# Kernel tuning notes

Hardware: AMD Instinct MI355X
Metric: run time of the kernel (lower is better)

The kernel has to match this reference:

```python
import jax, jax.numpy as jnp
import numpy as np

B, N, K, DEG = 512, 128, 8, 16
NR = 200            # num_rels (padding idx = NR)
INP, SEM, EMB, L = 32, 16, 32, 3
FEAT = INP - SEM
NN = B * N
E = NN * DEG
OUT = L * EMB       # 96


def _gru_cell(x, h, Wih, Whh, bih, bhh):
    gi = x @ Wih.T + bih
    gh = h @ Whh.T + bhh
    ir, iz, i_n = jnp.split(gi, 3, axis=-1)
    hr, hz, hn = jnp.split(gh, 3, axis=-1)
    r = jax.nn.sigmoid(ir + hr)
    z = jax.nn.sigmoid(iz + hz)
    n = jnp.tanh(i_n + r * hn)
    return (1.0 - z) * n + z * h


def _run_gru(xs, h0, Wih, Whh, bih, bhh):
    # xs: [T, batch, in]
    def step(h, x):
        h2 = _gru_cell(x, h, Wih, Whh, bih, bhh)
        return h2, h2
    hT, ys = jax.lax.scan(step, h0, xs)
    return ys, hT


def _forward(feat, out_nei_rels, in_nei_rels, r_label_node, src, dst, etype, rel_labels,
             rel_emb, w_rel2ent_W, w_rel2ent_b, W_msg, W_self, b_gnn, W_rel,
             gru_bias, gru_Wih_f, gru_Whh_f, gru_bih_f, gru_bhh_f,
             gru_Wih_b, gru_Whh_b, gru_bih_b, gru_bhh_b,
             Wo_W, Wo_b, path_Wih, path_Whh, path_bih, path_bhh, fc_W, fc_b):
    # --- init_ent_emb_matrix: neighbor-relation attention vs target relation ---
    out_e = rel_emb[out_nei_rels]                      # [NN,K,INP]
    in_e = rel_emb[in_nei_rels]                        # [NN,K,INP]
    tgt = rel_emb[r_label_node]                        # [NN,INP]
    out_att = jax.nn.softmax(jnp.einsum('nkd,nd->nk', out_e, tgt), axis=1)
    in_att = jax.nn.softmax(jnp.einsum('nkd,nd->nk', in_e, tgt), axis=1)
    out_sem = jnp.einsum('nk,nkd->nd', out_att, out_e)
    in_sem = jnp.einsum('nk,nkd->nd', in_att, in_e)
    sem = jax.nn.sigmoid(jnp.concatenate([out_sem, in_sem], axis=1) @ w_rel2ent_W + w_rel2ent_b)
    h = jnp.concatenate([feat, sem], axis=1)           # [NN,INP]

    # --- RGCN-style relational message passing; repr = concat of layer outputs ---
    r = rel_emb
    deg = jnp.maximum(jax.ops.segment_sum(jnp.ones((E,), h.dtype), dst, NN), 1.0)[:, None]
    reprs = []
    for l in range(L):
        msg = h[src] * r[etype]                        # [E,EMB]  (gather-heavy)
        agg = jax.ops.segment_sum(msg, dst, NN) / deg  # mean aggregation
        h = jax.nn.relu(agg @ W_msg[l] + h @ W_self[l] + b_gnn[l])
        r = r @ W_rel[l]                               # relation stream (padding row stays 0)
        reprs.append(h)
    repr_ = jnp.concatenate(reprs, axis=1)             # [NN,OUT]
    r_emb_out = r                                      # [NR+1,EMB]

    # --- BatchGRU: bidirectional GRU over each graph's node sequence ---
    node = repr_.reshape(B, N, OUT)
    message = jax.nn.relu(node + gru_bias)
    h0 = jnp.max(node, axis=1)                         # per-graph max init hidden
    xs = jnp.swapaxes(message, 0, 1)                   # [N,B,OUT]
    ys_f, _ = _run_gru(xs, h0, gru_Wih_f, gru_Whh_f, gru_bih_f, gru_bhh_f)
    ys_b, _ = _run_gru(xs[::-1], h0, gru_Wih_b, gru_Whh_b, gru_bih_b, gru_bhh_b)
    gru_out = jnp.concatenate([ys_f, ys_b[::-1]], axis=-1)  # [N,B,2*OUT]
    repr2 = jax.nn.relu(jnp.swapaxes(gru_out, 0, 1).reshape(NN, 2 * OUT))
    node_hidden = jax.nn.relu(repr2 @ Wo_W + Wo_b)     # [NN,OUT]

    nh = node_hidden.reshape(B, N, OUT)
    g_out = jnp.mean(nh, axis=1)                       # mean_nodes
    head_embs = nh[:, 0]                               # node id==1 is node 0 of each graph
    tail_embs = nh[:, 1]                               # node id==2 is node 1 of each graph

    # --- nei_rel_path: GRU over (h_r, r_t, t_r) triples, attention aggregation ---
    in_rels = in_nei_rels.reshape(B, N, K)
    heads_rels = in_rels[:, 0]                         # [B,K]
    tails_rels = in_rels[:, 1]                         # [B,K]
    P = K * K
    paths = jnp.stack([
        jnp.repeat(heads_rels, K, axis=1),
        jnp.broadcast_to(rel_labels[:, None], (B, P)),
        jnp.tile(tails_rels, (1, K)),
    ], axis=-1).reshape(B * P, 3)
    pe = r_emb_out[paths]                              # [B*P,3,EMB]
    _, last = _run_gru(jnp.swapaxes(pe, 0, 1), jnp.zeros((B * P, EMB), pe.dtype),
                       path_Wih, path_Whh, path_bih, path_bhh)
    last = last.reshape(B, P, EMB)
    r_lab_e = r_emb_out[rel_labels]                    # [B,EMB]
    atts = jax.nn.softmax(jnp.einsum('bpe,be->bp', last, r_lab_e), axis=1)
    g_p = jnp.einsum('bp,bpe->be', atts, last)         # [B,EMB]

    g_rep = jnp.concatenate([g_out, head_embs, tail_embs, r_lab_e, g_p], axis=1)  # [B,352]
    return g_rep @ fc_W + fc_b                         # [B,1]


def setup_inputs():
    key = jax.random.key(0)
    ks = jax.random.split(key, 40)
    idx = iter(range(40))
    def nk():
        return ks[next(idx)]
    def _p(shape, scale=0.1):
        return jax.random.normal(nk(), shape, jnp.float32) * scale

    feat = jax.random.normal(nk(), (NN, FEAT), jnp.float32)
    out_nei_rels = jax.random.randint(nk(), (NN, K), 0, NR)
    in_nei_rels = jax.random.randint(nk(), (NN, K), 0, NR)
    rel_labels = jax.random.randint(nk(), (B,), 0, NR)
    r_label_node = jnp.repeat(rel_labels, N)
    gid = jnp.arange(E) // (N * DEG)                   # edges stay within their graph
    src = gid * N + jax.random.randint(nk(), (E,), 0, N)
    dst = gid * N + jax.random.randint(nk(), (E,), 0, N)
    etype = jax.random.randint(nk(), (E,), 0, NR)
    rel_emb = jax.random.normal(nk(), (NR + 1, INP), jnp.float32) * 0.5
    rel_emb = rel_emb.at[NR].set(0.0)                  # padding_idx row

    return {
        'feat': feat, 'out_nei_rels': out_nei_rels, 'in_nei_rels': in_nei_rels,
        'r_label_node': r_label_node, 'src': src, 'dst': dst, 'etype': etype,
        'rel_labels': rel_labels, 'rel_emb': rel_emb,
        'w_rel2ent_W': _p((2 * INP, SEM)), 'w_rel2ent_b': _p((SEM,)),
        'W_msg': _p((L, EMB, EMB)), 'W_self': _p((L, EMB, EMB)),
        'b_gnn': _p((L, EMB)), 'W_rel': _p((L, INP, INP)),
        'gru_bias': _p((OUT,)),
        'gru_Wih_f': _p((3 * OUT, OUT)), 'gru_Whh_f': _p((3 * OUT, OUT)),
        'gru_bih_f': _p((3 * OUT,)), 'gru_bhh_f': _p((3 * OUT,)),
        'gru_Wih_b': _p((3 * OUT, OUT)), 'gru_Whh_b': _p((3 * OUT, OUT)),
        'gru_bih_b': _p((3 * OUT,)), 'gru_bhh_b': _p((3 * OUT,)),
        'Wo_W': _p((2 * OUT, OUT)), 'Wo_b': _p((OUT,)),
        'path_Wih': _p((3 * EMB, EMB)), 'path_Whh': _p((3 * EMB, EMB)),
        'path_bih': _p((3 * EMB,)), 'path_bhh': _p((3 * EMB,)),
        'fc_W': _p((3 * OUT + 2 * EMB, 1)), 'fc_b': _p((1,)),
    }


def reference(feat, out_nei_rels, in_nei_rels, r_label_node, src, dst, etype, rel_labels,
              rel_emb, w_rel2ent_W, w_rel2ent_b, W_msg, W_self, b_gnn, W_rel,
              gru_bias, gru_Wih_f, gru_Whh_f, gru_bih_f, gru_bhh_f,
              gru_Wih_b, gru_Whh_b, gru_bih_b, gru_bhh_b,
              Wo_W, Wo_b, path_Wih, path_Whh, path_bih, path_bhh, fc_W, fc_b):
    return _forward(feat, out_nei_rels, in_nei_rels, r_label_node, src, dst, etype, rel_labels,
                    rel_emb, w_rel2ent_W, w_rel2ent_b, W_msg, W_self, b_gnn, W_rel,
                    gru_bias, gru_Wih_f, gru_Whh_f, gru_bih_f, gru_bhh_f,
                    gru_Wih_b, gru_Whh_b, gru_bih_b, gru_bhh_b,
                    Wo_W, Wo_b, path_Wih, path_Whh, path_bih, path_bhh, fc_W, fc_b)
```

## Files before the change

### kernel.cpp

```cpp
#include <hip/hip_runtime.h>
#include <math.h>

#define BB 512
#define NT 128
#define NREL 201
#define NNODE (BB*NT)
#define NEDGE (NNODE*16)

typedef float f32x4 __attribute__((ext_vector_type(4)));
typedef __attribute__((ext_vector_type(8))) short bf16x8;

__device__ __forceinline__ float sigm(float x) { return 1.f/(1.f + __expf(-x)); }

__device__ __forceinline__ unsigned short f2bf(float f) {
  unsigned u; __builtin_memcpy(&u, &f, 4);
  unsigned r = u + 0x7fffu + ((u >> 16) & 1u);
  return (unsigned short)(r >> 16);
}

__global__ __launch_bounds__(96) void k_rel2(const float* __restrict__ rel_emb,
                                             const float* __restrict__ W_rel,
                                             const float* __restrict__ pWih,
                                             const float* __restrict__ pbih,
                                             float* __restrict__ r123,
                                             float* __restrict__ XI) {
  __shared__ float ra[32], rb[32];
  int r = blockIdx.x, tid = threadIdx.x;
  if (tid < 32) ra[tid] = rel_emb[r*32 + tid];
  __syncthreads();
  if (tid < 32) {
    float s = 0.f;
    #pragma unroll
    for (int d = 0; d < 32; ++d) s += ra[d]*W_rel[d*32 + tid];
    rb[tid] = s; r123[0*NREL*32 + r*32 + tid] = s;
  }
  __syncthreads();
  if (tid < 32) {
    float s = 0.f;
    #pragma unroll
    for (int d = 0; d < 32; ++d) s += rb[d]*W_rel[1024 + d*32 + tid];
    ra[tid] = s; r123[1*NREL*32 + r*32 + tid] = s;
  }
  __syncthreads();
  if (tid < 32) {
    float s = 0.f;
    #pragma unroll
    for (int d = 0; d < 32; ++d) s += ra[d]*W_rel[2048 + d*32 + tid];
    rb[tid] = s; r123[2*NREL*32 + r*32 + tid] = s;
  }
  __syncthreads();
  float s = pbih[tid];
  #pragma unroll
  for (int d = 0; d < 32; ++d) s += rb[d]*pWih[tid*32 + d];
  XI[r*96 + tid] = s;
}

__global__ __launch_bounds__(256) void k_wt1(const float* __restrict__ Wih_f,
                                             const float* __restrict__ Wih_b,
                                             const float* __restrict__ bih_f,
                                             const float* __restrict__ bih_b,
                                             unsigned short* __restrict__ WT1bt,
                                             float* __restrict__ bcat) {
  int i = blockIdx.x*256 + threadIdx.x;
  if (i < 576*96) {
    int j = i / 96;
    float v = (j < 288) ? Wih_f[i] : Wih_b[i - 288*96];
    WT1bt[i] = f2bf(v);
  }
  if (i < 576) bcat[i] = (i < 288) ? bih_f[i] : bih_b[i-288];
}

__device__ __forceinline__ void sem_att(const float* __restrict__ rel_emb,
                                        const int rels[8], const float tgt[32],
                                        float out[32]) {
  float dots[8]; float mx = -1e30f;
  #pragma unroll
  for (int k = 0; k < 8; ++k) {
    const float4* er = (const float4*)(rel_emb + rels[k]*32);
    float s = 0.f;
    #pragma unroll
    for (int q = 0; q < 8; ++q) {
      float4 v = er[q];
      s += v.x*tgt[4*q+0] + v.y*tgt[4*q+1] + v.z*tgt[4*q+2] + v.w*tgt[4*q+3];
    }
    dots[k] = s; mx = fmaxf(mx, s);
  }
  float den = 0.f;
  #pragma unroll
  for (int k = 0; k < 8; ++k) { float e = __expf(dots[k]-mx); dots[k] = e; den += e; }
  float inv = 1.f/den;
  #pragma unroll
  for (int d = 0; d < 32; ++d) out[d] = 0.f;
  #pragma unroll
  for (int k = 0; k < 8; ++k) {
    const float4* er = (const float4*)(rel_emb + rels[k]*32);
    float a = dots[k]*inv;
    #pragma unroll
    for (int q = 0; q < 8; ++q) {
      float4 v = er[q];
      out[4*q+0] += a*v.x; out[4*q+1] += a*v.y; out[4*q+2] += a*v.z; out[4*q+3] += a*v.w;
    }
  }
}

__global__ __launch_bounds__(256) void k_sem(
    const float* __restrict__ feat, const int* __restrict__ out_rels,
    const int* __restrict__ in_rels, const int* __restrict__ r_label_node,
    const float* __restrict__ rel_emb, const float* __restrict__ W,
    const float* __restrict__ bias, float* __restrict__ hin) {
  int n = blockIdx.x*256 + threadIdx.x;
  float tgt[32];
  {
    const float4* tr = (const float4*)(rel_emb + r_label_node[n]*32);
    #pragma unroll
    for (int q = 0; q < 8; ++q) {
      float4 v = tr[q];
      tgt[4*q+0]=v.x; tgt[4*q+1]=v.y; tgt[4*q+2]=v.z; tgt[4*q+3]=v.w;
    }
  }
  int ro[8], ri[8];
  #pragma unroll
  for (int k = 0; k < 8; ++k) { ro[k] = out_rels[n*8+k]; ri[k] = in_rels[n*8+k]; }
  float osem[32], isem[32];
  sem_att(rel_emb, ro, tgt, osem);
  sem_att(rel_emb, ri, tgt, isem);
  const float4* fr = (const float4*)(feat + (size_t)n*16);
  float4* ho = (float4*)(hin + (size_t)n*32);
  #pragma unroll
  for (int q = 0; q < 4; ++q) ho[q] = fr[q];
  #pragma unroll
  for (int j = 0; j < 16; ++j) {
    float s = bias[j];
    #pragma unroll
    for (int d = 0; d < 32; ++d) s += osem[d]*W[d*16+j] + isem[d]*W[(32+d)*16+j];
    hin[(size_t)n*32 + 16 + j] = sigm(s);
  }
}

__global__ __launch_bounds__(512) void k_gnn3(
    const float* __restrict__ hin, const float* __restrict__ rel_emb,
    const float* __restrict__ r123,
    const int* __restrict__ src, const int* __restrict__ dst, const int* __restrict__ etype,
    const float* __restrict__ W_msg, const float* __restrict__ W_self,
    const float* __restrict__ b_gnn,
    float* __restrict__ AT, float* __restrict__ ghid0) {
  __shared__ __align__(16) float hl[NT*36];
  __shared__ __align__(16) float hnew[NT*33];
  __shared__ float rl[NREL*32];
  __shared__ unsigned short eidx[2048];
  __shared__ float scratch[16][32];
  __shared__ int cnt[128], fill[128], scanv[128], rowstart[129];
  int g = blockIdx.x;
  int tid = threadIdx.x;
  int d = tid & 31, grp = tid >> 5;

  for (int i = tid; i < NT*32; i += 512) {
    int row = i >> 5, col = i & 31;
    hl[row*36 + col] = hin[(size_t)(g*NT + row)*32 + col];
  }
  if (tid < 128) { cnt[tid] = 0; fill[tid] = 0; }
  __syncthreads();
  for (int i = tid; i < 2048; i += 512)
    atomicAdd(&cnt[dst[g*2048 + i] - g*NT], 1);
  __syncthreads();
  if (tid < 128) scanv[tid] = cnt[tid];
  __syncthreads();
  #pragma unroll
  for (int off = 1; off < 128; off <<= 1) {
    int v = 0;
    if (tid < 128 && tid >= off) v = scanv[tid - off];
    __syncthreads();
    if (tid < 128) scanv[tid] += v;
    __syncthreads();
  }
  if (tid < 128) { rowstart[tid+1] = scanv[tid]; if (tid == 0) rowstart[0] = 0; }
  __syncthreads();
  for (int i = tid; i < 2048; i += 512) {
    int e = g*2048 + i;
    int dl = dst[e] - g*NT;
    int slot = rowstart[dl] + atomicAdd(&fill[dl], 1);
    eidx[slot] = (unsigned short)(((src[e] - g*NT) << 8) | etype[e]);
  }

  for (int l = 0; l < 3; ++l) {
    const float* rsrc = (l == 0) ? rel_emb : (r123 + (size_t)(l-1)*NREL*32);
    for (int i = tid; i < NREL*32; i += 512) rl[i] = rsrc[i];
    float wm[32], ws[32];
    #pragma unroll
    for (int dd = 0; dd < 32; ++dd) {
      wm[dd] = W_msg[l*1024 + dd*32 + d];
      ws[dd] = W_self[l*1024 + dd*32 + d];
    }
    float bj = b_gnn[l*32 + d];
    __syncthreads();
    for (int k2 = 0; k2 < 8; ++k2) {
      int n = grp + k2*16;
      int e0 = rowstart[n], e1 = rowstart[n+1];
      float acc = 0.f;
      for (int e = e0; e < e1; ++e) {
        int pk = eidx[e];
        acc += hl[(pk >> 8)*36 + d] * rl[(pk & 255)*32 + d];
      }
      scratch[grp][d] = acc;
      float invd = 1.f / (float)((e1 - e0) > 0 ? (e1 - e0) : 1);
      float sa = 0.f, sh = 0.f;
      #pragma unroll
      for (int dd = 0; dd < 32; ++dd) {
        sa += scratch[grp][dd]*wm[dd];
        sh += hl[n*36 + dd]*ws[dd];
      }
      hnew[n*33 + d] = fmaxf(bj + invd*sa + sh, 0.f);
    }
    __syncthreads();
    for (int i = tid; i < NT*32; i += 512) {
      int row = i >> 5, col = i & 31;
      hl[row*36 + col] = hnew[row*33 + col];
    }
    #pragma unroll
    for (int pass = 0; pass < 8; ++pass) {
      int col = (pass << 2) + (tid >> 7);
      int row = tid & 127;
      AT[(size_t)(l*32 + col)*NNODE + g*NT + row] = hnew[row*33 + col];
    }
    {
      float m = -1e30f;
      #pragma unroll
      for (int k2 = 0; k2 < 8; ++k2) m = fmaxf(m, hnew[(grp + k2*16)*33 + d]);
      scratch[grp][d] = m;
    }
    __syncthreads();
    if (tid < 32) {
      float m = -1e30f;
      #pragma unroll
      for (int p2 = 0; p2 < 16; ++p2) m = fmaxf(m, scratch[p2][tid]);
      ghid0[g*96 + l*32 + tid] = m;
    }
    __syncthreads();
  }
}

__global__ __launch_bounds__(256) void k_gemm1m(
    const float* __restrict__ AT, const float* __restrict__ gbias,
    const unsigned short* __restrict__ WT1bt, const float* __restrict__ bcat,
    float* __restrict__ GI) {
  __shared__ unsigned short As[128*104];
  int m0 = blockIdx.x * 128;
  int tid = threadIdx.x;
  for (int i = tid; i < 96*32; i += 256) {
    int r = i >> 5, c4 = i & 31;
    float4 v = *(const float4*)&AT[(size_t)r*NNODE + m0 + c4*4];
    float b = gbias[r];
    float o0 = fmaxf(v.x+b,0.f), o1 = fmaxf(v.y+b,0.f);
    float o2 = fmaxf(v.z+b,0.f), o3 = fmaxf(v.w+b,0.f);
    As[(c4*4+0)*104 + r] = f2bf(o0);
    As[(c4*4+1)*104 + r] = f2bf(o1);
    As[(c4*4+2)*104 + r] = f2bf(o2);
    As[(c4*4+3)*104 + r] = f2bf(o3);
  }
  __syncthreads();
  int w = tid >> 6, l = tid & 63;
  int lr = l & 15, lh = l >> 4;
  bf16x8 afr[2][3];
  #pragma unroll
  for (int tm = 0; tm < 2; ++tm)
    #pragma unroll
    for (int kc = 0; kc < 3; ++kc)
      afr[tm][kc] = *(const bf16x8*)&As[((w*2+tm)*16 + lr)*104 + kc*32 + lh*8];
  for (int nb = 0; nb < 9; ++nb) {
    int n0 = nb*64;
    #pragma unroll
    for (int tn = 0; tn < 4; ++tn) {
      int col = n0 + tn*16 + lr;
      const unsigned short* bp = WT1bt + (size_t)col*96 + lh*8;
      bf16x8 b0 = *(const bf16x8*)(bp);
      bf16x8 b1 = *(const bf16x8*)(bp + 32);
      bf16x8 b2 = *(const bf16x8*)(bp + 64);
      float bb = bcat[col];
      #pragma unroll
      for (int tm = 0; tm < 2; ++tm) {
        f32x4 acc = {bb, bb, bb, bb};
        acc = __builtin_amdgcn_mfma_f32_16x16x32_bf16(afr[tm][0], b0, acc, 0, 0, 0);
        acc = __builtin_amdgcn_mfma_f32_16x16x32_bf16(afr[tm][1], b1, acc, 0, 0, 0);
        acc = __builtin_amdgcn_mfma_f32_16x16x32_bf16(afr[tm][2], b2, acc, 0, 0, 0);
        int rbase = m0 + (w*2+tm)*16 + lh*4;
        #pragma unroll
        for (int r = 0; r < 4; ++r)
          __builtin_nontemporal_store(acc[r], &GI[(size_t)(rbase + r)*576 + col]);
      }
    }
  }
}

#define PIN4(v) asm volatile("" : "+v"(v.x), "+v"(v.y), "+v"(v.z), "+v"(v.w))
#define DOT16(acc, W0,W1,W2,W3, X0,X1,X2,X3) \
  acc += W0.x*X0.x + W0.y*X0.y + W0.z*X0.z + W0.w*X0.w \
       + W1.x*X1.x + W1.y*X1.y + W1.z*X1.z + W1.w*X1.w \
       + W2.x*X2.x + W2.y*X2.y + W2.z*X2.z + W2.w*X2.w \
       + W3.x*X3.x + W3.y*X3.y + W3.z*X3.z + W3.w*X3.w

__global__ __launch_bounds__(576, 1) void k_gru(
    const float* __restrict__ Whh_f, const float* __restrict__ bhh_f,
    const float* __restrict__ Whh_b, const float* __restrict__ bhh_b,
    const float* __restrict__ GI, const float* __restrict__ ghid0,
    float* __restrict__ AT2) {
  __shared__ __align__(16) float h_lds[4][96];
  __shared__ float part[4][288][9];
  int bx = blockIdx.x;
  int dir = bx >> 7;
  int gbase = (bx & 127) * 4;
  int tid = threadIdx.x;
  int c = tid % 96;
  int p = tid / 96;
  bool fin = (tid < 384);
  int s = p;

  const float* Whh = dir ? Whh_b : Whh_f;
  const float4* wr0 = (const float4*)(Whh + (size_t)c*96 + p*16);
  const float4* wr1 = (const float4*)(Whh + (size_t)(96+c)*96 + p*16);
  const float4* wr2 = (const float4*)(Whh + (size_t)(192+c)*96 + p*16);
  float4 wa0=wr0[0], wa1=wr0[1], wa2=wr0[2], wa3=wr0[3];
  float4 wb0=wr1[0], wb1=wr1[1], wb2=wr1[2], wb3=wr1[3];
  float4 wc0=wr2[0], wc1=wr2[1], wc2=wr2[2], wc3=wr2[3];

  float bh0=0.f, bh1=0.f, bh2=0.f;
  float gi0=0.f, gi1=0.f, gi2=0.f;
  if (fin) {
    const float* bhh = dir ? bhh_b : bhh_f;
    bh0 = bhh[c]; bh1 = bhh[96+c]; bh2 = bhh[192+c];
    h_lds[s][c] = ghid0[(gbase+s)*96 + c];
    int pos0 = dir ? 127 : 0;
    const float* g = GI + (size_t)((gbase+s)*128 + pos0)*576 + dir*288;
    gi0 = g[c]; gi1 = g[96+c]; gi2 = g[192+c];
  }
  __syncthreads();
  for (int t = 0; t < 128; ++t) {
    PIN4(wa0); PIN4(wa1); PIN4(wa2); PIN4(wa3);
    PIN4(wb0); PIN4(wb1); PIN4(wb2); PIN4(wb3);
    PIN4(wc0); PIN4(wc1); PIN4(wc2); PIN4(wc3);
    int pos = dir ? (127-t) : t;
    float gn0=0.f, gn1=0.f, gn2=0.f;
    if (fin && t < 127) {
      int posn = dir ? (126-t) : (t+1);
      const float* g = GI + (size_t)((gbase+s)*128 + posn)*576 + dir*288;
      gn0 = g[c]; gn1 = g[96+c]; gn2 = g[192+c];
    }
    #pragma unroll
    for (int s4 = 0; s4 < 4; ++s4) {
      const float4* hh = (const float4*)&h_lds[s4][p*16];
      float4 x0=hh[0], x1=hh[1], x2=hh[2], x3=hh[3];
      float q0=0.f, q1=0.f, q2=0.f;
      DOT16(q0, wa0,wa1,wa2,wa3, x0,x1,x2,x3);
      DOT16(q1, wb0,wb1,wb2,wb3, x0,x1,x2,x3);
      DOT16(q2, wc0,wc1,wc2,wc3, x0,x1,x2,x3);
      part[s4][c][p]     = q0;
      part[s4][96+c][p]  = q1;
      part[s4][192+c][p] = q2;
    }
    __syncthreads();
    if (fin) {
      const float* pr = part[s][c];
      const float* pz = part[s][96+c];
      const float* pn = part[s][192+c];
      float ghr = pr[0]+pr[1]+pr[2]+pr[3]+pr[4]+pr[5] + bh0;
      float ghz = pz[0]+pz[1]+pz[2]+pz[3]+pz[4]+pz[5] + bh1;
      float ghn = pn[0]+pn[1]+pn[2]+pn[3]+pn[4]+pn[5] + bh2;
      float r  = sigm(gi0 + ghr);
      float z  = sigm(gi1 + ghz);
      float nn = tanhf(gi2 + r*ghn);
      float hv = (1.f - z)*nn + z*h_lds[s][c];
      h_lds[s][c] = hv;
      AT2[(size_t)(dir*96 + c)*NNODE + (gbase+s)*128 + pos] = fmaxf(hv, 0.f);
      gi0 = gn0; gi1 = gn1; gi2 = gn2;
    }
    __syncthreads();
  }
}

__global__ __launch_bounds__(384) void k_gemm2p(
    const float* __restrict__ AT2, const float* __restrict__ WoW,
    const float* __restrict__ Wob, float* __restrict__ goutb,
    float* __restrict__ headb, float* __restrict__ tailb) {
  __shared__ __align__(16) float As[96*64];
  __shared__ __align__(16) float Bs[96*96];
  __shared__ float red[16][100];
  int m0 = blockIdx.x*64;
  int g = m0 >> 7;
  int tid = threadIdx.x;
  int tc = tid % 24, tr = tid / 24;
  int r0 = tr*4, c0 = tc*4;
  float acc[4][4] = {};
  for (int kc = 0; kc < 2; ++kc) {
    for (int i = tid; i < 1536; i += 384) {
      int r = i >> 4, c4 = i & 15;
      *(float4*)&As[r*64 + c4*4] = *(const float4*)&AT2[(size_t)(kc*96 + r)*NNODE + m0 + c4*4];
    }
    for (int i = tid; i < 2304; i += 384) {
      int r = i / 24, c4 = i % 24;
      *(float4*)&Bs[r*96 + c4*4] = *(const float4*)&WoW[(size_t)(kc*96 + r)*96 + c4*4];
    }
    __syncthreads();
    #pragma unroll 8
    for (int k = 0; k < 96; ++k) {
      float4 a = *(float4*)&As[k*64 + r0];
      float4 b = *(float4*)&Bs[k*96 + c0];
      acc[0][0] += a.x*b.x; acc[0][1] += a.x*b.y; acc[0][2] += a.x*b.z; acc[0][3] += a.x*b.w;
      acc[1][0] += a.y*b.x; acc[1][1] += a.y*b.y; acc[1][2] += a.y*b.z; acc[1][3] += a.y*b.w;
      acc[2][0] += a.z*b.x; acc[2][1] += a.z*b.y; acc[2][2] += a.z*b.z; acc[2][3] += a.z*b.w;
      acc[3][0] += a.w*b.x; acc[3][1] += a.w*b.y; acc[3][2] += a.w*b.z; acc[3][3] += a.w*b.w;
    }
    __syncthreads();
  }
  float4 bia = *(const float4*)&Wob[c0];
  float nv[4][4];
  #pragma unroll
  for (int r = 0; r < 4; ++r) {
    nv[r][0] = fmaxf(acc[r][0]+bia.x, 0.f);
    nv[r][1] = fmaxf(acc[r][1]+bia.y, 0.f);
    nv[r][2] = fmaxf(acc[r][2]+bia.z, 0.f);
    nv[r][3] = fmaxf(acc[r][3]+bia.w, 0.f);
  }
  #pragma unroll
  for (int cj = 0; cj < 4; ++cj)
    red[tr][c0+cj] = nv[0][cj] + nv[1][cj] + nv[2][cj] + nv[3][cj];
  if ((m0 & 127) == 0 && tr == 0) {
    #pragma unroll
    for (int cj = 0; cj < 4; ++cj) {
      headb[g*96 + c0 + cj] = nv[0][cj];
      tailb[g*96 + c0 + cj] = nv[1][cj];
    }
  }
  __syncthreads();
  if (tid < 96) {
    float s = 0.f;
    #pragma unroll
    for (int t2 = 0; t2 < 16; ++t2) s += red[t2][tid];
    atomicAdd(&goutb[g*96 + tid], s);
  }
}

__global__ __launch_bounds__(128) void k_path(
    const float* __restrict__ XI, const int* __restrict__ in_rels,
    const int* __restrict__ labels, const float* __restrict__ pWhh,
    const float* __restrict__ pbhh, float* __restrict__ last) {
  __shared__ __align__(16) float wsh[96*32];
  __shared__ float bsh[96];
  __shared__ float hbuf[128*33];
  int tid = threadIdx.x;
  for (int i = tid; i < 96*32; i += 128) wsh[i] = pWhh[i];
  if (tid < 96) bsh[tid] = pbhh[tid];
  int p = blockIdx.x*128 + tid;
  int b = p >> 6, pp = p & 63;
  int rid0 = in_rels[b*1024 + (pp >> 3)];
  int rid1 = labels[b];
  int rid2 = in_rels[b*1024 + 8 + (pp & 7)];
  __syncthreads();
  float* hs = &hbuf[tid*33];
  {
    const float* xi = XI + rid0*96;
    #pragma unroll
    for (int gg = 0; gg < 32; ++gg) {
      float r = sigm(xi[gg] + bsh[gg]);
      float z = sigm(xi[32+gg] + bsh[32+gg]);
      float nn = tanhf(xi[64+gg] + r*bsh[64+gg]);
      hs[gg] = (1.f - z)*nn;
    }
  }
  float4 h4[8];
  #pragma unroll
  for (int q = 0; q < 8; ++q) h4[q] = make_float4(hs[4*q], hs[4*q+1], hs[4*q+2], hs[4*q+3]);
  for (int s = 0; s < 2; ++s) {
    const float* xi = XI + (s == 0 ? rid1 : rid2)*96;
    for (int gg = 0; gg < 32; ++gg) {
      float ar = bsh[gg], az = bsh[32+gg], an = bsh[64+gg];
      const float4* wr = (const float4*)&wsh[gg*32];
      const float4* wz = (const float4*)&wsh[(32+gg)*32];
      const float4* wn = (const float4*)&wsh[(64+gg)*32];
      #pragma unroll
      for (int q = 0; q < 8; ++q) {
        float4 hv = h4[q]; float4 w;
        w = wr[q]; ar += hv.x*w.x + hv.y*w.y + hv.z*w.z + hv.w*w.w;
        w = wz[q]; az += hv.x*w.x + hv.y*w.y + hv.z*w.z + hv.w*w.w;
        w = wn[q]; an += hv.x*w.x + hv.y*w.y + hv.z*w.z + hv.w*w.w;
      }
      float r = sigm(xi[gg] + ar);
      float z = sigm(xi[32+gg] + az);
      float nn = tanhf(xi[64+gg] + r*an);
      hs[gg] = (1.f - z)*nn + z*hs[gg];
    }
    #pragma unroll
    for (int q = 0; q < 8; ++q) h4[q] = make_float4(hs[4*q], hs[4*q+1], hs[4*q+2], hs[4*q+3]);
  }
  float* lp = last + (size_t)p*32;
  #pragma unroll
  for (int d = 0; d < 32; ++d) lp[d] = hs[d];
}

__global__ __launch_bounds__(64) void k_final(
    const float* __restrict__ last, const float* __restrict__ r3,
    const int* __restrict__ labels, const float* __restrict__ goutb,
    const float* __restrict__ headb, const float* __restrict__ tailb,
    const float* __restrict__ fcW, const float* __restrict__ fcb,
    float* __restrict__ out) {
  __shared__ float red[64*33];
  __shared__ float gpl[32];
  int b = blockIdx.x, lane = threadIdx.x;
  const float* rl = r3 + labels[b]*32;
  float l32[32];
  {
    const float4* lr = (const float4*)(last + (size_t)(b*64 + lane)*32);
    #pragma unroll
    for (int q = 0; q < 8; ++q) {
      float4 v = lr[q];
      l32[4*q+0]=v.x; l32[4*q+1]=v.y; l32[4*q+2]=v.z; l32[4*q+3]=v.w;
    }
  }
  float s = 0.f;
  #pragma unroll
  for (int d = 0; d < 32; ++d) s += l32[d]*rl[d];
  float mx = s;
  #pragma unroll
  for (int off = 32; off > 0; off >>= 1) mx = fmaxf(mx, __shfl_xor(mx, off));
  float e = __expf(s - mx);
  float den = e;
  #pragma unroll
  for (int off = 32; off > 0; off >>= 1) den += __shfl_xor(den, off);
  float att = e / den;
  #pragma unroll
  for (int d = 0; d < 32; ++d) red[lane*33 + d] = att*l32[d];
  __syncthreads();
  if (lane < 32) {
    float gp = 0.f;
    for (int p2 = 0; p2 < 64; ++p2) gp += red[p2*33 + lane];
    gpl[lane] = gp;
  }
  __syncthreads();
  float acc = 0.f;
  for (int i = lane; i < 352; i += 64) {
    float v;
    if (i < 96)       v = goutb[b*96 + i] * 0.0078125f;
    else if (i < 192) v = headb[b*96 + (i-96)];
    else if (i < 288) v = tailb[b*96 + (i-192)];
    else if (i < 320) v = rl[i-288];
    else              v = gpl[i-320];
    acc += v*fcW[i];
  }
  #pragma unroll
  for (int off = 32; off > 0; off >>= 1) acc += __shfl_xor(acc, off);
  if (lane == 0) out[b] = acc + fcb[0];
}

extern "C" void kernel_launch(void* const* d_in, const int* in_sizes, int n_in,
                              void* d_out, int out_size, void* d_ws, size_t ws_size,
                              hipStream_t stream) {
  const float* feat       = (const float*)d_in[0];
  const int*   out_rels   = (const int*)d_in[1];
  const int*   in_rels    = (const int*)d_in[2];
  const int*   r_label_nd = (const int*)d_in[3];
  const int*   src        = (const int*)d_in[4];
  const int*   dst        = (const int*)d_in[5];
  const int*   etype      = (const int*)d_in[6];
  const int*   rel_labels = (const int*)d_in[7];
  const float* rel_emb    = (const float*)d_in[8];
  const float* w2e_W      = (const float*)d_in[9];
  const float* w2e_b      = (const float*)d_in[10];
  const float* W_msg      = (const float*)d_in[11];
  const float* W_self     = (const float*)d_in[12];
  const float* b_gnn      = (const float*)d_in[13];
  const float* W_rel      = (const float*)d_in[14];
  const float* gru_bias   = (const float*)d_in[15];
  const float* Wih_f      = (const float*)d_in[16];
  const float* Whh_f      = (const float*)d_in[17];
  const float* bih_f      = (const float*)d_in[18];
  const float* bhh_f      = (const float*)d_in[19];
  const float* Wih_b      = (const float*)d_in[20];
  const float* Whh_b      = (const float*)d_in[21];
  const float* bih_b      = (const float*)d_in[22];
  const float* bhh_b      = (const float*)d_in[23];
  const float* Wo_W       = (const float*)d_in[24];
  const float* Wo_b       = (const float*)d_in[25];
  const float* pWih       = (const float*)d_in[26];
  const float* pWhh       = (const float*)d_in[27];
  const float* pbih       = (const float*)d_in[28];
  const float* pbhh       = (const float*)d_in[29];
  const float* fcW        = (const float*)d_in[30];
  const float* fcb        = (const float*)d_in[31];
  float* out = (float*)d_out;

  float* p = (float*)d_ws;
  float* hin   = p; p += (size_t)NNODE*32;
  float* R1    = p; p += (size_t)NNODE*192;
  float* AT    = R1;
  float* AT2   = R1;
  float* R2    = p; p += (size_t)NNODE*576;
  float* GI    = R2;
  float* r123  = p; p += 3*NREL*32;
  unsigned short* WT1bt = (unsigned short*)p; p += (576*96)/2;
  float* bcat  = p; p += 576;
  float* XI    = p; p += NREL*96;
  float* ghid0 = p; p += BB*96;
  float* goutb = p; p += BB*96;
  float* headb = p; p += BB*96;
  float* tailb = p; p += BB*96;
  float* lastb = p; p += (size_t)BB*64*32;

  hipMemsetAsync(goutb, 0, BB*96*sizeof(float), stream);
  k_rel2<<<NREL, 96, 0, stream>>>(rel_emb, W_rel, pWih, pbih, r123, XI);
  k_wt1<<<(576*96+255)/256, 256, 0, stream>>>(Wih_f, Wih_b, bih_f, bih_b, WT1bt, bcat);
  k_sem<<<NNODE/256, 256, 0, stream>>>(feat, out_rels, in_rels, r_label_nd,
                                       rel_emb, w2e_W, w2e_b, hin);
  k_gnn3<<<BB, 512, 0, stream>>>(hin, rel_emb, r123, src, dst, etype,
                                 W_msg, W_self, b_gnn, AT, ghid0);
  k_gemm1m<<<512, 256, 0, stream>>>(AT, gru_bias, WT1bt, bcat, GI);
  k_gru<<<256, 576, 0, stream>>>(Whh_f, bhh_f, Whh_b, bhh_b, GI, ghid0, AT2);
  k_gemm2p<<<1024, 384, 0, stream>>>(AT2, Wo_W, Wo_b, goutb, headb, tailb);
  k_path<<<256, 128, 0, stream>>>(XI, in_rels, rel_labels, pWhh, pbhh, lastb);
  k_final<<<BB, 64, 0, stream>>>(lastb, r123 + 2*NREL*32, rel_labels,
                                 goutb, headb, tailb, fcW, fcb, out);
}
```

Baseline: 504.0 us.

## Run GRU recurrence on MFMA with split-bf16 weights and interleaved gate layout

The bidirectional GRU hidden-state matmul moves from scalar FP32 dot products with an LDS partial-sum reduction to bf16 MFMA instructions. Weights and hidden state are split into hi/lo bf16 pairs (three MFMA passes) to keep near-FP32 accuracy. The input-gate GEMM now writes its outputs with the r/z/n gates interleaved per channel, so each lane loads all three with one vector load. Each block now handles 16 sequences instead of 4, giving 64 blocks instead of 256. That removes one barrier per step but leaves most CUs idle and adds a weight-prep kernel.

```diff
diff --git a/kernel.cpp b/kernel.cpp
--- a/kernel.cpp
+++ b/kernel.cpp
@@ -16,6 +16,11 @@
   unsigned u; __builtin_memcpy(&u, &f, 4);
   unsigned r = u + 0x7fffu + ((u >> 16) & 1u);
   return (unsigned short)(r >> 16);
+}
+__device__ __forceinline__ float bf2f(unsigned short h) {
+  unsigned u = ((unsigned)h) << 16;
+  float f; __builtin_memcpy(&f, &u, 4);
+  return f;
 }
 
 __global__ __launch_bounds__(96) void k_rel2(const float* __restrict__ rel_emb,
@@ -68,6 +73,27 @@
     WT1bt[i] = f2bf(v);
   }
   if (i < 576) bcat[i] = (i < 288) ? bih_f[i] : bih_b[i-288];
+}
+
+__global__ __launch_bounds__(256) void k_wprep(const float* __restrict__ Whh_f,
+                                               const float* __restrict__ Whh_b,
+                                               unsigned short* __restrict__ WhhP) {
+  int i = blockIdx.x*256 + threadIdx.x;
+  if (i >= 2*384*96) return;
+  int dir = i / (384*96);
+  int rem = i - dir*384*96;
+  int row = rem / 96, k = rem - (rem/96)*96;
+  int c = row >> 2, g = row & 3;
+  float w = 0.f;
+  if (g < 3) {
+    const float* W = dir ? Whh_b : Whh_f;
+    w = W[(size_t)(g*96 + c)*96 + k];
+  }
+  unsigned short hi = f2bf(w);
+  unsigned short lo = f2bf(w - bf2f(hi));
+  size_t base = (size_t)dir*2*384*96;
+  WhhP[base + rem] = hi;
+  WhhP[base + 384*96 + rem] = lo;
 }
 
 __device__ __forceinline__ void sem_att(const float* __restrict__ rel_emb,
@@ -250,12 +276,10 @@
     int r = i >> 5, c4 = i & 31;
     float4 v = *(const float4*)&AT[(size_t)r*NNODE + m0 + c4*4];
     float b = gbias[r];
-    float o0 = fmaxf(v.x+b,0.f), o1 = fmaxf(v.y+b,0.f);
-    float o2 = fmaxf(v.z+b,0.f), o3 = fmaxf(v.w+b,0.f);
-    As[(c4*4+0)*104 + r] = f2bf(o0);
-    As[(c4*4+1)*104 + r] = f2bf(o1);
-    As[(c4*4+2)*104 + r] = f2bf(o2);
-    As[(c4*4+3)*104 + r] = f2bf(o3);
+    As[(c4*4+0)*104 + r] = f2bf(fmaxf(v.x+b,0.f));
+    As[(c4*4+1)*104 + r] = f2bf(fmaxf(v.y+b,0.f));
+    As[(c4*4+2)*104 + r] = f2bf(fmaxf(v.z+b,0.f));
+    As[(c4*4+3)*104 + r] = f2bf(fmaxf(v.w+b,0.f));
   }
   __syncthreads();
   int w = tid >> 6, l = tid & 63;
@@ -271,6 +295,11 @@
     #pragma unroll
     for (int tn = 0; tn < 4; ++tn) {
       int col = n0 + tn*16 + lr;
+      int dirv = (col >= 288) ? 1 : 0;
+      int rr = col - dirv*288;
+      int gate = (rr >= 192) ? 2 : (rr >= 96 ? 1 : 0);
+      int cch = rr - gate*96;
+      int jp = dirv*288 + cch*3 + gate;
       const unsigned short* bp = WT1bt + (size_t)col*96 + lh*8;
       bf16x8 b0 = *(const bf16x8*)(bp);
       bf16x8 b1 = *(const bf16x8*)(bp + 32);
@@ -285,94 +314,104 @@
         int rbase = m0 + (w*2+tm)*16 + lh*4;
         #pragma unroll
         for (int r = 0; r < 4; ++r)
-          __builtin_nontemporal_store(acc[r], &GI[(size_t)(rbase + r)*576 + col]);
+          __builtin_nontemporal_store(acc[r], &GI[(size_t)(rbase + r)*576 + jp]);
       }
     }
   }
 }
 
-#define PIN4(v) asm volatile("" : "+v"(v.x), "+v"(v.y), "+v"(v.z), "+v"(v.w))
-#define DOT16(acc, W0,W1,W2,W3, X0,X1,X2,X3) \
-  acc += W0.x*X0.x + W0.y*X0.y + W0.z*X0.z + W0.w*X0.w \
-       + W1.x*X1.x + W1.y*X1.y + W1.z*X1.z + W1.w*X1.w \
-       + W2.x*X2.x + W2.y*X2.y + W2.z*X2.z + W2.w*X2.w \
-       + W3.x*X3.x + W3.y*X3.y + W3.z*X3.z + W3.w*X3.w
-
-__global__ __launch_bounds__(576, 1) void k_gru(
-    const float* __restrict__ Whh_f, const float* __restrict__ bhh_f,
-    const float* __restrict__ Whh_b, const float* __restrict__ bhh_b,
+#define PINV(x) asm volatile("" : "+v"(x))
+
+__global__ __launch_bounds__(512, 2) void k_gru(
+    const unsigned short* __restrict__ WhhP,
+    const float* __restrict__ bhh_f, const float* __restrict__ bhh_b,
     const float* __restrict__ GI, const float* __restrict__ ghid0,
     float* __restrict__ AT2) {
-  __shared__ __align__(16) float h_lds[4][96];
-  __shared__ float part[4][288][9];
-  int bx = blockIdx.x;
-  int dir = bx >> 7;
-  int gbase = (bx & 127) * 4;
+  __shared__ unsigned short hbuf[2][2][16][104];
+  int b = blockIdx.x;
+  int dir = b >> 5;
+  int G = (b & 31) * 16;
   int tid = threadIdx.x;
-  int c = tid % 96;
-  int p = tid / 96;
-  bool fin = (tid < 384);
-  int s = p;
-
-  const float* Whh = dir ? Whh_b : Whh_f;
-  const float4* wr0 = (const float4*)(Whh + (size_t)c*96 + p*16);
-  const float4* wr1 = (const float4*)(Whh + (size_t)(96+c)*96 + p*16);
-  const float4* wr2 = (const float4*)(Whh + (size_t)(192+c)*96 + p*16);
-  float4 wa0=wr0[0], wa1=wr0[1], wa2=wr0[2], wa3=wr0[3];
-  float4 wb0=wr1[0], wb1=wr1[1], wb2=wr1[2], wb3=wr1[3];
-  float4 wc0=wr2[0], wc1=wr2[1], wc2=wr2[2], wc3=wr2[3];
-
-  float bh0=0.f, bh1=0.f, bh2=0.f;
-  float gi0=0.f, gi1=0.f, gi2=0.f;
-  if (fin) {
-    const float* bhh = dir ? bhh_b : bhh_f;
-    bh0 = bhh[c]; bh1 = bhh[96+c]; bh2 = bhh[192+c];
-    h_lds[s][c] = ghid0[(gbase+s)*96 + c];
-    int pos0 = dir ? 127 : 0;
-    const float* g = GI + (size_t)((gbase+s)*128 + pos0)*576 + dir*288;
-    gi0 = g[c]; gi1 = g[96+c]; gi2 = g[192+c];
-  }
-  __syncthreads();
+  int w = tid >> 6, l = tid & 63;
+  int s = l & 15, q = l >> 4;
+  const float* bhh = dir ? bhh_b : bhh_f;
+
+  bf16x8 Ahi[3][3], Alo[3][3];
+  const unsigned short* WP = WhhP + (size_t)dir*2*384*96;
+  int cj[3];
+  float bhr[3], bhz[3], bhn[3], hreg[3];
+  #pragma unroll
+  for (int j = 0; j < 3; ++j) {
+    int t = 3*w + j;
+    int row = t*16 + s;
+    #pragma unroll
+    for (int kc = 0; kc < 3; ++kc) {
+      Ahi[j][kc] = *(const bf16x8*)&WP[(size_t)row*96 + kc*32 + q*8];
+      Alo[j][kc] = *(const bf16x8*)&WP[(size_t)(384*96) + (size_t)row*96 + kc*32 + q*8];
+    }
+    cj[j] = 12*w + 4*j + q;
+    bhr[j] = bhh[cj[j]]; bhz[j] = bhh[96+cj[j]]; bhn[j] = bhh[192+cj[j]];
+    float h0 = ghid0[(G+s)*96 + cj[j]];
+    hreg[j] = h0;
+    unsigned short hi = f2bf(h0);
+    hbuf[0][0][s][cj[j]] = hi;
+    hbuf[0][1][s][cj[j]] = f2bf(h0 - bf2f(hi));
+  }
+  int node_s = (G + s)*128;
+  int pos0 = dir ? 127 : 0;
+  f32x4 gi[3];
+  #pragma unroll
+  for (int j = 0; j < 3; ++j)
+    gi[j] = *(const f32x4*)&GI[(size_t)(node_s + pos0)*576 + dir*288 + cj[j]*3];
+  __syncthreads();
+
+  int cur = 0;
   for (int t = 0; t < 128; ++t) {
-    PIN4(wa0); PIN4(wa1); PIN4(wa2); PIN4(wa3);
-    PIN4(wb0); PIN4(wb1); PIN4(wb2); PIN4(wb3);
-    PIN4(wc0); PIN4(wc1); PIN4(wc2); PIN4(wc3);
+    #pragma unroll
+    for (int j = 0; j < 3; ++j) {
+      #pragma unroll
+      for (int kc = 0; kc < 3; ++kc) { PINV(Ahi[j][kc]); PINV(Alo[j][kc]); }
+    }
     int pos = dir ? (127-t) : t;
-    float gn0=0.f, gn1=0.f, gn2=0.f;
-    if (fin && t < 127) {
+    bf16x8 Bhi[3], Blo[3];
+    #pragma unroll
+    for (int kc = 0; kc < 3; ++kc) {
+      Bhi[kc] = *(const bf16x8*)&hbuf[cur][0][s][kc*32 + q*8];
+      Blo[kc] = *(const bf16x8*)&hbuf[cur][1][s][kc*32 + q*8];
+    }
+    f32x4 gn[3];
+    if (t < 127) {
       int posn = dir ? (126-t) : (t+1);
-      const float* g = GI + (size_t)((gbase+s)*128 + posn)*576 + dir*288;
-      gn0 = g[c]; gn1 = g[96+c]; gn2 = g[192+c];
-    }
-    #pragma unroll
-    for (int s4 = 0; s4 < 4; ++s4) {
-      const float4* hh = (const float4*)&h_lds[s4][p*16];
-      float4 x0=hh[0], x1=hh[1], x2=hh[2], x3=hh[3];
-      float q0=0.f, q1=0.f, q2=0.f;
-      DOT16(q0, wa0,wa1,wa2,wa3, x0,x1,x2,x3);
-      DOT16(q1, wb0,wb1,wb2,wb3, x0,x1,x2,x3);
-      DOT16(q2, wc0,wc1,wc2,wc3, x0,x1,x2,x3);
-      part[s4][c][p]     = q0;
-      part[s4][96+c][p]  = q1;
-      part[s4][192+c][p] = q2;
-    }
-    __syncthreads();
-    if (fin) {
-      const float* pr = part[s][c];
-      const float* pz = part[s][96+c];
-      const float* pn = part[s][192+c];
-      float ghr = pr[0]+pr[1]+pr[2]+pr[3]+pr[4]+pr[5] + bh0;
-      float ghz = pz[0]+pz[1]+pz[2]+pz[3]+pz[4]+pz[5] + bh1;
-      float ghn = pn[0]+pn[1]+pn[2]+pn[3]+pn[4]+pn[5] + bh2;
-      float r  = sigm(gi0 + ghr);
-      float z  = sigm(gi1 + ghz);
-      float nn = tanhf(gi2 + r*ghn);
-      float hv = (1.f - z)*nn + z*h_lds[s][c];
-      h_lds[s][c] = hv;
-      AT2[(size_t)(dir*96 + c)*NNODE + (gbase+s)*128 + pos] = fmaxf(hv, 0.f);
-      gi0 = gn0; gi1 = gn1; gi2 = gn2;
-    }
-    __syncthreads();
+      #pragma unroll
+      for (int j = 0; j < 3; ++j)
+        gn[j] = *(const f32x4*)&GI[(size_t)(node_s + posn)*576 + dir*288 + cj[j]*3];
+    } else {
+      #pragma unroll
+      for (int j = 0; j < 3; ++j) gn[j] = gi[j];
+    }
+    #pragma unroll
+    for (int j = 0; j < 3; ++j) {
+      f32x4 acc = {0.f, 0.f, 0.f, 0.f};
+      #pragma unroll
+      for (int kc = 0; kc < 3; ++kc) acc = __builtin_amdgcn_mfma_f32_16x16x32_bf16(Ahi[j][kc], Bhi[kc], acc, 0, 0, 0);
+      #pragma unroll
+      for (int kc = 0; kc < 3; ++kc) acc = __builtin_amdgcn_mfma_f32_16x16x32_bf16(Ahi[j][kc], Blo[kc], acc, 0, 0, 0);
+      #pragma unroll
+      for (int kc = 0; kc < 3; ++kc) acc = __builtin_amdgcn_mfma_f32_16x16x32_bf16(Alo[j][kc], Bhi[kc], acc, 0, 0, 0);
+      float r  = sigm(gi[j].x + acc[0] + bhr[j]);
+      float z  = sigm(gi[j].y + acc[1] + bhz[j]);
+      float nn = tanhf(gi[j].z + r*(acc[2] + bhn[j]));
+      float hv = (1.f - z)*nn + z*hreg[j];
+      hreg[j] = hv;
+      unsigned short hi = f2bf(hv);
+      hbuf[cur^1][0][s][cj[j]] = hi;
+      hbuf[cur^1][1][s][cj[j]] = f2bf(hv - bf2f(hi));
+      AT2[(size_t)(dir*96 + cj[j])*NNODE + node_s + pos] = fmaxf(hv, 0.f);
+    }
+    #pragma unroll
+    for (int j = 0; j < 3; ++j) gi[j] = gn[j];
+    __syncthreads();
+    cur ^= 1;
   }
 }
 
@@ -591,10 +630,11 @@
   float* R1    = p; p += (size_t)NNODE*192;
   float* AT    = R1;
   float* AT2   = R1;
-  float* R2    = p; p += (size_t)NNODE*576;
+  float* R2    = p; p += (size_t)NNODE*576 + 16;
   float* GI    = R2;
   float* r123  = p; p += 3*NREL*32;
   unsigned short* WT1bt = (unsigned short*)p; p += (576*96)/2;
+  unsigned short* WhhP  = (unsigned short*)p; p += (2*2*384*96)/2;
   float* bcat  = p; p += 576;
   float* XI    = p; p += NREL*96;
   float* ghid0 = p; p += BB*96;
@@ -606,12 +646,13 @@
   hipMemsetAsync(goutb, 0, BB*96*sizeof(float), stream);
   k_rel2<<<NREL, 96, 0, stream>>>(rel_emb, W_rel, pWih, pbih, r123, XI);
   k_wt1<<<(576*96+255)/256, 256, 0, stream>>>(Wih_f, Wih_b, bih_f, bih_b, WT1bt, bcat);
+  k_wprep<<<(2*384*96+255)/256, 256, 0, stream>>>(Whh_f, Whh_b, WhhP);
   k_sem<<<NNODE/256, 256, 0, stream>>>(feat, out_rels, in_rels, r_label_nd,
                                        rel_emb, w2e_W, w2e_b, hin);
   k_gnn3<<<BB, 512, 0, stream>>>(hin, rel_emb, r123, src, dst, etype,
                                  W_msg, W_self, b_gnn, AT, ghid0);
   k_gemm1m<<<512, 256, 0, stream>>>(AT, gru_bias, WT1bt, bcat, GI);
-  k_gru<<<256, 576, 0, stream>>>(Whh_f, bhh_f, Whh_b, bhh_b, GI, ghid0, AT2);
+  k_gru<<<64, 512, 0, stream>>>(WhhP, bhh_f, bhh_b, GI, ghid0, AT2);
   k_gemm2p<<<1024, 384, 0, stream>>>(AT2, Wo_W, Wo_b, goutb, headb, tailb);
   k_path<<<256, 128, 0, stream>>>(XI, in_rels, rel_labels, pWhh, pbhh, lastb);
   k_final<<<BB, 64, 0, stream>>>(lastb, r123 + 2*NREL*32, rel_labels,
```

Result: slower. 771.0 us (+53.0%).
